# Performance work log

Hardware: AMD Instinct MI355X
Metric: run time of the kernel (lower is better)

Reference implementation:

```python
import jax, jax.numpy as jnp
import numpy as np

B, S, H, K, L, NH, FF = 4, 2048, 2048, 1024, 2, 16, 4096
EPS = 1e-5

def _alibi_slopes(n):
    # standard power-of-two ALiBi slopes
    start = 2.0 ** (-8.0 / n)
    return start ** jnp.arange(1, n + 1, dtype=jnp.float32)

def _layernorm(h, g, b):
    mu = jnp.mean(h, axis=-1, keepdims=True)
    var = jnp.mean(jnp.square(h - mu), axis=-1, keepdims=True)
    return (h - mu) * jax.lax.rsqrt(var + EPS) * g + b

def setup_inputs() -> dict:
    key = jax.random.key(0)
    ks = jax.random.split(key, 16)
    x = jax.random.normal(ks[0], (B, S, H), jnp.float32)
    prev = jax.random.normal(ks[1], (B, S, H), jnp.float32)
    # unique sorted token indices per batch row (jit-friendly boolean mask)
    idx = jnp.stack([jnp.sort(jax.random.permutation(jax.random.fold_in(ks[2], b), S)[:K])
                     for b in range(B)]).astype(jnp.int32)
    w = 0.02
    Wq = jax.random.normal(ks[3], (L, H, H), jnp.float32) * w
    Wk = jax.random.normal(ks[4], (L, H, H), jnp.float32) * w
    Wv = jax.random.normal(ks[5], (L, H, H), jnp.float32) * w
    Wo = jax.random.normal(ks[6], (L, H, H), jnp.float32) * w
    attn_gamma = jnp.ones((L, H), jnp.float32)
    attn_beta = jnp.zeros((L, H), jnp.float32)
    mlp_gamma = jnp.ones((L, H), jnp.float32)
    mlp_beta = jnp.zeros((L, H), jnp.float32)
    Wgate = jax.random.normal(ks[7], (L, H, FF), jnp.float32) * w
    Wup = jax.random.normal(ks[8], (L, H, FF), jnp.float32) * w
    Wdown = jax.random.normal(ks[9], (L, FF, H), jnp.float32) * w
    return {"x": x, "prev": prev, "idx": idx, "Wq": Wq, "Wk": Wk, "Wv": Wv,
            "Wo": Wo, "attn_gamma": attn_gamma, "attn_beta": attn_beta,
            "mlp_gamma": mlp_gamma, "mlp_beta": mlp_beta,
            "Wgate": Wgate, "Wup": Wup, "Wdown": Wdown}

def _forward(x, prev, idx, Wq, Wk, Wv, Wo, attn_gamma, attn_beta,
             mlp_gamma, mlp_beta, Wgate, Wup, Wdown):
    d = H // NH
    scale = 1.0 / jnp.sqrt(jnp.asarray(d, jnp.float32))
    # gather selected tokens: [B, K, H]
    cur = jnp.take_along_axis(x, idx[:, :, None], axis=1)
    mem = jnp.take_along_axis(prev, idx[:, :, None], axis=1)
    # non-causal ALiBi bias over selected-sequence positions: [NH, K, K]
    pos = jnp.arange(K)
    dist = jnp.abs(pos[:, None] - pos[None, :]).astype(jnp.float32)
    bias = -_alibi_slopes(NH)[:, None, None] * dist
    for l in range(L):
        q = (cur @ Wq[l]).reshape(B, K, NH, d)
        k = (mem @ Wk[l]).reshape(B, K, NH, d)
        v = (mem @ Wv[l]).reshape(B, K, NH, d)
        scores = jnp.einsum('bqhd,bkhd->bhqk', q, k) * scale + bias
        attn = jax.nn.softmax(scores, axis=-1)
        o = jnp.einsum('bhqk,bkhd->bqhd', attn, v).reshape(B, K, H) @ Wo[l]
        cur = cur + o
        normed = _layernorm(cur, attn_gamma[l], attn_beta[l])
        mlp = (jax.nn.silu(normed @ Wgate[l]) * (normed @ Wup[l])) @ Wdown[l]
        cur = cur + mlp
        cur = _layernorm(cur, mlp_gamma[l], mlp_beta[l])
    # scatter-add back: out[mask] += update_val
    out = x.at[jnp.arange(B)[:, None], idx].add(cur)
    return out

def reference(x, prev, idx, Wq, Wk, Wv, Wo, attn_gamma, attn_beta,
              mlp_gamma, mlp_beta, Wgate, Wup, Wdown):
    return _forward(x, prev, idx, Wq, Wk, Wv, Wo, attn_gamma, attn_beta,
                    mlp_gamma, mlp_beta, Wgate, Wup, Wdown)
```

## Files before the change

kernel.cpp:

```cpp
#include <hip/hip_runtime.h>
#include <hip/hip_bf16.h>

#define BB 4
#define SS 2048
#define HH 2048
#define KK 1024
#define LL 2
#define NHH 16
#define FFF 4096
#define DD 128

typedef __attribute__((ext_vector_type(8))) short s8v;
typedef __attribute__((ext_vector_type(4))) short s4v;
typedef __attribute__((ext_vector_type(4))) float f4v;

__device__ __forceinline__ short f2bf(float f) {
  unsigned u = __builtin_bit_cast(unsigned, f);
  u += 0x7fffu + ((u >> 16) & 1u);
  return (short)(u >> 16);
}
__device__ __forceinline__ float bf2f(short s) {
  unsigned u = ((unsigned)(unsigned short)s) << 16;
  return __builtin_bit_cast(float, u);
}
__device__ __forceinline__ f4v mfma16(s8v a, s8v b, f4v c) {
  asm("v_mfma_f32_16x16x32_bf16 %0, %1, %2, %0" : "+v"(c) : "v"(a), "v"(b));
  return c;
}
__device__ __forceinline__ void gload_lds16(const void* g, void* l) {
  __builtin_amdgcn_global_load_lds(
      (__attribute__((address_space(1))) void*)g,
      (__attribute__((address_space(3))) void*)l, 16, 0, 0);
}
template <int N>
__device__ __forceinline__ void barrier_cnt() {
  if constexpr (N == 3)
    asm volatile("s_waitcnt vmcnt(3) expcnt(0) lgkmcnt(0)" ::: "memory");
  else
    asm volatile("s_waitcnt vmcnt(0) expcnt(0) lgkmcnt(0)" ::: "memory");
  __builtin_amdgcn_s_barrier();
  asm volatile("" ::: "memory");
}

__global__ __launch_bounds__(256) void wconv(const float* __restrict__ W,
                                             short* __restrict__ Wt,
                                             int Kd, int N) {
  __shared__ short tile[64][65];
  int n0 = blockIdx.x * 64, k0 = blockIdx.y * 64;
  int t = threadIdx.x;
#pragma unroll
  for (int i = 0; i < 16; ++i) {
    int lin = i * 256 + t;
    int r = lin >> 6, c = lin & 63;
    tile[c][r] = f2bf(W[(size_t)(k0 + r) * N + n0 + c]);
  }
  __syncthreads();
#pragma unroll
  for (int i = 0; i < 16; ++i) {
    int lin = i * 256 + t;
    int r = lin >> 6, c = lin & 63;
    Wt[(size_t)(n0 + r) * Kd + k0 + c] = tile[r][c];
  }
}

__global__ __launch_bounds__(256) void gather_rows(
    const float* __restrict__ x, const float* __restrict__ prev,
    const int* __restrict__ idx, float* __restrict__ cur_f,
    short* __restrict__ cur_b, short* __restrict__ mem_b) {
  int r = blockIdx.x;
  int b = r >> 10, kk = r & (KK - 1);
  int src = idx[b * KK + kk];
  const float4* xs = (const float4*)(x + ((size_t)b * SS + src) * HH);
  const float4* ps = (const float4*)(prev + ((size_t)b * SS + src) * HH);
  float4* cf = (float4*)(cur_f + (size_t)r * HH);
  s4v* cb = (s4v*)(cur_b + (size_t)r * HH);
  s4v* mb = (s4v*)(mem_b + (size_t)r * HH);
  int t = threadIdx.x;
#pragma unroll
  for (int i = 0; i < 2; ++i) {
    int c = t + i * 256;
    float4 xv = xs[c], pv = ps[c];
    cf[c] = xv;
    s4v cv, mv;
    cv[0] = f2bf(xv.x); cv[1] = f2bf(xv.y); cv[2] = f2bf(xv.z); cv[3] = f2bf(xv.w);
    mv[0] = f2bf(pv.x); mv[1] = f2bf(pv.y); mv[2] = f2bf(pv.z); mv[3] = f2bf(pv.w);
    cb[c] = cv; mb[c] = mv;
  }
}

template <int EPI>
__global__ __launch_bounds__(512, 2) void g8p(
    const short* __restrict__ A, const short* __restrict__ Bt,
    float* __restrict__ Cf, short* __restrict__ Cb,
    const short* __restrict__ Other, int M, int N, int Kd) {
  __shared__ __align__(16) short smem[3 * 12288];
  const int t = threadIdx.x;
  const int w = t >> 6, l = t & 63;
  const int wr = w >> 2, wc = w & 3;
  const int l15 = l & 15, lh = l >> 4;
  const int koffs = (lh ^ ((l15 >> 1) & 3)) * 8;

  const int gx = gridDim.x, gy = gridDim.y;
  const int nwg = gx * gy;
  const int bid = blockIdx.y * gx + blockIdx.x;
  const int wg = (bid & 7) * (nwg >> 3) + (bid >> 3);
  const int by = wg & (gy - 1);
  const int bx = wg / gy;
  const int rowBase = by * 128, colBase = bx * 256;

  const int ar = t >> 2;
  const int ac = ((t & 3) ^ ((t >> 3) & 3)) * 8;
  const short* gA = A + (size_t)(rowBase + ar) * Kd + ac;
  const short* gB0 = Bt + (size_t)(colBase + ar) * Kd + ac;
  const short* gB1 = gB0 + (size_t)128 * Kd;
  const int lA = t * 8;
  const int lB = 4096 + t * 8;

  auto stage = [&](int bi, int kt) {
    const int k0 = kt * 32;
    short* base = smem + bi * 12288;
    gload_lds16(gA + k0, base + lA);
    gload_lds16(gB0 + k0, base + lB);
    gload_lds16(gB1 + k0, base + lB + 4096);
  };

  f4v acc[4][4];
#pragma unroll
  for (int i = 0; i < 4; ++i)
#pragma unroll
    for (int j = 0; j < 4; ++j) acc[i][j] = (f4v){0.f, 0.f, 0.f, 0.f};

  const int NT = Kd >> 5;
  stage(0, 0);
  stage(1, 1);
  barrier_cnt<3>();

  int cur = 0;
  for (int kt = 0; kt < NT; ++kt) {
    const short* sb = smem + cur * 12288;
    const bool more = (kt + 2 < NT);
    if (more) {
      int nb = cur + 2; if (nb >= 3) nb -= 3;
      stage(nb, kt + 2);
    }
    s8v af[4], bf[4];
#pragma unroll
    for (int mt = 0; mt < 4; ++mt)
      af[mt] = *(const s8v*)(sb + (wr * 64 + mt * 16 + l15) * 32 + koffs);
#pragma unroll
    for (int nt = 0; nt < 4; ++nt)
      bf[nt] = *(const s8v*)(sb + 4096 + (wc * 64 + nt * 16 + l15) * 32 + koffs);
#pragma unroll
    for (int mt = 0; mt < 4; ++mt)
#pragma unroll
      for (int nt = 0; nt < 4; ++nt)
        acc[mt][nt] = mfma16(af[mt], bf[nt], acc[mt][nt]);
    if (more) barrier_cnt<3>(); else barrier_cnt<0>();
    cur = (cur + 1 == 3) ? 0 : cur + 1;
  }

#pragma unroll
  for (int mt = 0; mt < 4; ++mt) {
#pragma unroll
    for (int nt = 0; nt < 4; ++nt) {
#pragma unroll
      for (int rr = 0; rr < 4; ++rr) {
        int row = rowBase + wr * 64 + mt * 16 + (l >> 4) * 4 + rr;
        int col = colBase + wc * 64 + nt * 16 + l15;
        float v = acc[mt][nt][rr];
        if constexpr (EPI == 0) {
          Cb[(size_t)row * N + col] = f2bf(v);
        } else if constexpr (EPI == 1) {
          Cf[(size_t)row * N + col] += v;
        } else if constexpr (EPI == 2) {
          int b = row >> 10, ktok = row & (KK - 1);
          int h = col >> 7, dd = col & (DD - 1);
          Cb[(((size_t)(b * NHH + h)) * DD + dd) * KK + ktok] = f2bf(v);
        } else if constexpr (EPI == 3) {
          float sv = v / (1.f + __expf(-v));
          Cb[(size_t)row * N + col] = f2bf(sv);
        } else {
          float o = bf2f(Other[(size_t)row * N + col]);
          Cb[(size_t)row * N + col] = f2bf(v * o);
        }
      }
    }
  }
}

__global__ __launch_bounds__(256, 2) void attn_fwd(
    const short* __restrict__ qb, const short* __restrict__ kb,
    const short* __restrict__ vT, short* __restrict__ ob) {
  __shared__ __align__(16) short Kl[64 * 136];
  __shared__ __align__(16) short Vl[128 * 72];
  __shared__ __align__(16) short Pl[64 * 72];
  int b = blockIdx.z, h = blockIdx.y, qt = blockIdx.x;
  int t = threadIdx.x, w = t >> 6, l = t & 63, l15 = l & 15, lh = l >> 4;
  float slope = exp2f(-0.5f * (float)(h + 1));
  const float scale = 0.08838834764831845f;

  s8v qf[4];
  int qrowA = qt * 64 + w * 16 + l15;
  const short* qptr = qb + ((size_t)(b * KK + qrowA)) * HH + h * DD + lh * 8;
#pragma unroll
  for (int ks = 0; ks < 4; ++ks) qf[ks] = *(const s8v*)(qptr + ks * 32);

  f4v oacc[8];
#pragma unroll
  for (int i = 0; i < 8; ++i) oacc[i] = (f4v){0.f, 0.f, 0.f, 0.f};
  float m[4], sden[4];
#pragma unroll
  for (int r = 0; r < 4; ++r) { m[r] = -1e30f; sden[r] = 0.f; }
  int qpos_base = qt * 64 + w * 16 + lh * 4;

  for (int kt = 0; kt < KK / 64; ++kt) {
    {
      int rr = t >> 4, cc = (t & 15) * 8;
#pragma unroll
      for (int it = 0; it < 4; ++it) {
        int krow = it * 16 + rr;
        s8v g = *(const s8v*)(kb + ((size_t)(b * KK + kt * 64 + krow)) * HH + h * DD + cc);
        *(s8v*)&Kl[krow * 136 + cc] = g;
      }
      int dr = t >> 3, c2 = (t & 7) * 8;
#pragma unroll
      for (int it = 0; it < 4; ++it) {
        int drow = it * 32 + dr;
        s8v g = *(const s8v*)(vT + (((size_t)(b * NHH + h)) * DD + drow) * KK + kt * 64 + c2);
        *(s8v*)&Vl[drow * 72 + c2] = g;
      }
    }
    __syncthreads();

    f4v sacc[4];
#pragma unroll
    for (int ct = 0; ct < 4; ++ct) sacc[ct] = (f4v){0.f, 0.f, 0.f, 0.f};
#pragma unroll
    for (int ct = 0; ct < 4; ++ct)
#pragma unroll
      for (int ks = 0; ks < 4; ++ks) {
        s8v kf = *(const s8v*)&Kl[(ct * 16 + l15) * 136 + ks * 32 + lh * 8];
        sacc[ct] = mfma16(qf[ks], kf, sacc[ct]);
      }

#pragma unroll
    for (int r = 0; r < 4; ++r) {
      int qpos = qpos_base + r;
      float mx = -1e30f;
#pragma unroll
      for (int ct = 0; ct < 4; ++ct) {
        int kpos = kt * 64 + ct * 16 + l15;
        float sv = sacc[ct][r] * scale - slope * fabsf((float)(qpos - kpos));
        sacc[ct][r] = sv;
        mx = fmaxf(mx, sv);
      }
      mx = fmaxf(mx, __shfl_xor(mx, 1));
      mx = fmaxf(mx, __shfl_xor(mx, 2));
      mx = fmaxf(mx, __shfl_xor(mx, 4));
      mx = fmaxf(mx, __shfl_xor(mx, 8));
      float mn = fmaxf(m[r], mx);
      float corr = __expf(m[r] - mn);
      m[r] = mn;
      float ps = 0.f;
#pragma unroll
      for (int ct = 0; ct < 4; ++ct) {
        float p = __expf(sacc[ct][r] - mn);
        sacc[ct][r] = p;
        ps += p;
      }
      ps += __shfl_xor(ps, 1); ps += __shfl_xor(ps, 2);
      ps += __shfl_xor(ps, 4); ps += __shfl_xor(ps, 8);
      sden[r] = sden[r] * corr + ps;
#pragma unroll
      for (int dt = 0; dt < 8; ++dt) oacc[dt][r] *= corr;
#pragma unroll
      for (int ct = 0; ct < 4; ++ct)
        Pl[(w * 16 + lh * 4 + r) * 72 + ct * 16 + l15] = f2bf(sacc[ct][r]);
    }

#pragma unroll
    for (int ks2 = 0; ks2 < 2; ++ks2) {
      s8v pa = *(const s8v*)&Pl[(w * 16 + l15) * 72 + ks2 * 32 + lh * 8];
#pragma unroll
      for (int dt = 0; dt < 8; ++dt) {
        s8v vf = *(const s8v*)&Vl[(dt * 16 + l15) * 72 + ks2 * 32 + lh * 8];
        oacc[dt] = mfma16(pa, vf, oacc[dt]);
      }
    }
    __syncthreads();
  }

#pragma unroll
  for (int dt = 0; dt < 8; ++dt)
#pragma unroll
    for (int r = 0; r < 4; ++r) {
      int qpos = qpos_base + r;
      int dd = dt * 16 + l15;
      ob[((size_t)(b * KK + qpos)) * HH + h * DD + dd] = f2bf(oacc[dt][r] / sden[r]);
    }
}

__global__ __launch_bounds__(256) void ln_rows(const float* in,
    const float* __restrict__ gma, const float* __restrict__ bta,
    short* __restrict__ outb, float* outf) {
  __shared__ float red[2][4];
  int r = blockIdx.x, t = threadIdx.x;
  const float4* x4 = (const float4*)(in + (size_t)r * HH);
  float4 va = x4[t], vb = x4[t + 256];
  float sum = va.x + va.y + va.z + va.w + vb.x + vb.y + vb.z + vb.w;
  float sq = va.x * va.x + va.y * va.y + va.z * va.z + va.w * va.w +
             vb.x * vb.x + vb.y * vb.y + vb.z * vb.z + vb.w * vb.w;
#pragma unroll
  for (int off = 32; off; off >>= 1) {
    sum += __shfl_down(sum, off);
    sq += __shfl_down(sq, off);
  }
  int w = t >> 6;
  if ((t & 63) == 0) { red[0][w] = sum; red[1][w] = sq; }
  __syncthreads();
  sum = red[0][0] + red[0][1] + red[0][2] + red[0][3];
  sq = red[1][0] + red[1][1] + red[1][2] + red[1][3];
  float mu = sum * (1.f / HH);
  float rs = rsqrtf(sq * (1.f / HH) - mu * mu + 1e-5f);
  const float4* g4 = (const float4*)gma;
  const float4* b4 = (const float4*)bta;
  s4v* ob = (s4v*)(outb + (size_t)r * HH);
  float4* of = (float4*)(outf ? outf + (size_t)r * HH : nullptr);
#pragma unroll
  for (int i = 0; i < 2; ++i) {
    int c = t + i * 256;
    float4 v = (i == 0) ? va : vb;
    float4 g = g4[c], bb = b4[c];
    float4 nv;
    nv.x = (v.x - mu) * rs * g.x + bb.x;
    nv.y = (v.y - mu) * rs * g.y + bb.y;
    nv.z = (v.z - mu) * rs * g.z + bb.z;
    nv.w = (v.w - mu) * rs * g.w + bb.w;
    s4v o;
    o[0] = f2bf(nv.x); o[1] = f2bf(nv.y); o[2] = f2bf(nv.z); o[3] = f2bf(nv.w);
    ob[c] = o;
    if (outf) of[c] = nv;
  }
}

__global__ __launch_bounds__(256) void copy_out(const float* __restrict__ x,
                                                float* __restrict__ out, size_t n4) {
  size_t i = (size_t)blockIdx.x * 256 + threadIdx.x;
  size_t stride = (size_t)gridDim.x * 256;
  const float4* xi = (const float4*)x;
  float4* oi = (float4*)out;
  for (; i < n4; i += stride) oi[i] = xi[i];
}

__global__ __launch_bounds__(256) void scatter_add(const int* __restrict__ idx,
                                                   const float* __restrict__ cur,
                                                   float* out) {
  int r = blockIdx.x;
  int b = r >> 10, kk = r & (KK - 1);
  int dst = idx[b * KK + kk];
  float4* o = (float4*)(out + ((size_t)b * SS + dst) * HH);
  const float4* c = (const float4*)(cur + (size_t)r * HH);
  int t = threadIdx.x;
#pragma unroll
  for (int i = 0; i < 2; ++i) {
    int j = t + i * 256;
    float4 ov = o[j], cv = c[j];
    ov.x += cv.x; ov.y += cv.y; ov.z += cv.z; ov.w += cv.w;
    o[j] = ov;
  }
}

extern "C" void kernel_launch(void* const* d_in, const int* in_sizes, int n_in,
                              void* d_out, int out_size, void* d_ws, size_t ws_size,
                              hipStream_t stream) {
  (void)in_sizes; (void)n_in; (void)out_size; (void)ws_size;
  const float* x = (const float*)d_in[0];
  const float* prv = (const float*)d_in[1];
  const int* idx = (const int*)d_in[2];
  const float* Wq = (const float*)d_in[3];
  const float* Wk = (const float*)d_in[4];
  const float* Wv = (const float*)d_in[5];
  const float* Wo = (const float*)d_in[6];
  const float* ag = (const float*)d_in[7];
  const float* ab = (const float*)d_in[8];
  const float* mg = (const float*)d_in[9];
  const float* mbt = (const float*)d_in[10];
  const float* Wg = (const float*)d_in[11];
  const float* Wu = (const float*)d_in[12];
  const float* Wd = (const float*)d_in[13];
  float* out = (float*)d_out;

  char* ws = (char*)d_ws;
  size_t off = 0;
  auto alloc = [&](size_t bytes) -> void* {
    void* p = ws + off;
    off += (bytes + 255) & ~(size_t)255;
    return p;
  };
  const size_t WHH = (size_t)HH * HH, WHF = (size_t)HH * FFF;
  short* WqT = (short*)alloc(LL * WHH * 2);
  short* WkT = (short*)alloc(LL * WHH * 2);
  short* WvT = (short*)alloc(LL * WHH * 2);
  short* WoT = (short*)alloc(LL * WHH * 2);
  short* WgT = (short*)alloc(LL * WHF * 2);
  short* WuT = (short*)alloc(LL * WHF * 2);
  short* WdT = (short*)alloc(LL * WHF * 2);
  const size_t RH = (size_t)BB * KK * HH;
  float* cur_f = (float*)alloc(RH * 4);
  short* q_b = (short*)alloc(RH * 2);
  short* k_b = (short*)alloc(RH * 2);
  short* vT_b = (short*)alloc(RH * 2);
  short* o_b = (short*)alloc(RH * 2);
  short* cur_b = (short*)alloc(RH * 2);
  short* mem_b = (short*)alloc(RH * 2);
  short* nrm_b = (short*)alloc(RH * 2);
  short* sg_b = q_b;
  short* hid_b = vT_b;

  dim3 blk(256), blk512(512);
  for (int l = 0; l < LL; ++l) {
    wconv<<<dim3(HH / 64, HH / 64), blk, 0, stream>>>(Wq + l * WHH, WqT + l * WHH, HH, HH);
    wconv<<<dim3(HH / 64, HH / 64), blk, 0, stream>>>(Wk + l * WHH, WkT + l * WHH, HH, HH);
    wconv<<<dim3(HH / 64, HH / 64), blk, 0, stream>>>(Wv + l * WHH, WvT + l * WHH, HH, HH);
    wconv<<<dim3(HH / 64, HH / 64), blk, 0, stream>>>(Wo + l * WHH, WoT + l * WHH, HH, HH);
    wconv<<<dim3(FFF / 64, HH / 64), blk, 0, stream>>>(Wg + l * WHF, WgT + l * WHF, HH, FFF);
    wconv<<<dim3(FFF / 64, HH / 64), blk, 0, stream>>>(Wu + l * WHF, WuT + l * WHF, HH, FFF);
    wconv<<<dim3(HH / 64, FFF / 64), blk, 0, stream>>>(Wd + l * WHF, WdT + l * WHF, FFF, HH);
  }
  gather_rows<<<dim3(BB * KK), blk, 0, stream>>>(x, prv, idx, cur_f, cur_b, mem_b);

  const int M = BB * KK;
  for (int l = 0; l < LL; ++l) {
    const short* wq = WqT + l * WHH;
    const short* wk = WkT + l * WHH;
    const short* wv = WvT + l * WHH;
    const short* wo = WoT + l * WHH;
    const short* wg_ = WgT + l * WHF;
    const short* wu = WuT + l * WHF;
    const short* wd = WdT + l * WHF;
    g8p<0><<<dim3(HH / 256, M / 128), blk512, 0, stream>>>(cur_b, wq, nullptr, q_b, nullptr, M, HH, HH);
    g8p<0><<<dim3(HH / 256, M / 128), blk512, 0, stream>>>(mem_b, wk, nullptr, k_b, nullptr, M, HH, HH);
    g8p<2><<<dim3(HH / 256, M / 128), blk512, 0, stream>>>(mem_b, wv, nullptr, vT_b, nullptr, M, HH, HH);
    attn_fwd<<<dim3(KK / 64, NHH, BB), blk, 0, stream>>>(q_b, k_b, vT_b, o_b);
    g8p<1><<<dim3(HH / 256, M / 128), blk512, 0, stream>>>(o_b, wo, cur_f, nullptr, nullptr, M, HH, HH);
    ln_rows<<<dim3(M), blk, 0, stream>>>(cur_f, ag + l * HH, ab + l * HH, nrm_b, nullptr);
    g8p<3><<<dim3(FFF / 256, M / 128), blk512, 0, stream>>>(nrm_b, wg_, nullptr, sg_b, nullptr, M, FFF, HH);
    g8p<4><<<dim3(FFF / 256, M / 128), blk512, 0, stream>>>(nrm_b, wu, nullptr, hid_b, sg_b, M, FFF, HH);
    g8p<1><<<dim3(HH / 256, M / 128), blk512, 0, stream>>>(hid_b, wd, cur_f, nullptr, nullptr, M, HH, FFF);
    ln_rows<<<dim3(M), blk, 0, stream>>>(cur_f, mg + l * HH, mbt + l * HH, cur_b, cur_f);
  }
  copy_out<<<dim3(2048), blk, 0, stream>>>(x, out, (size_t)BB * SS * HH / 4);
  scatter_add<<<dim3(M), blk, 0, stream>>>(idx, cur_f, out);
}
```

Before: 1.338 ms.

## Add 256x256-tile GEMM for MLP gate/up and lazy-rescale exp2 softmax in attention

Adds a new GEMM kernel with 256x256 output tiles, a three-buffer global-to-LDS pipeline and a remapped workgroup order, and uses it for the two large FFN up-projections. The larger tile is meant to raise arithmetic intensity and cut global and LDS traffic per MFMA, at the cost of more accumulator registers and LDS. Separately, the attention kernel folds log2(e) into the scale and ALiBi slope so it can use exp2, and skips the running-max rescale of the output and denominator when every lane's new max is within 8 of the old one. That skip saves multiplies but allows unrescaled exponents up to 2^8, which is a small numerical risk.

After: 1.448 ms. 8.3% more time.

```diff
diff --git a/kernel.cpp b/kernel.cpp
--- a/kernel.cpp
+++ b/kernel.cpp
@@ -36,6 +36,8 @@
 __device__ __forceinline__ void barrier_cnt() {
   if constexpr (N == 3)
     asm volatile("s_waitcnt vmcnt(3) expcnt(0) lgkmcnt(0)" ::: "memory");
+  else if constexpr (N == 4)
+    asm volatile("s_waitcnt vmcnt(4) expcnt(0) lgkmcnt(0)" ::: "memory");
   else
     asm volatile("s_waitcnt vmcnt(0) expcnt(0) lgkmcnt(0)" ::: "memory");
   __builtin_amdgcn_s_barrier();
@@ -165,7 +167,7 @@
     for (int nt = 0; nt < 4; ++nt) {
 #pragma unroll
       for (int rr = 0; rr < 4; ++rr) {
-        int row = rowBase + wr * 64 + mt * 16 + (l >> 4) * 4 + rr;
+        int row = rowBase + wr * 64 + mt * 16 + lh * 4 + rr;
         int col = colBase + wc * 64 + nt * 16 + l15;
         float v = acc[mt][nt][rr];
         if constexpr (EPI == 0) {
@@ -188,6 +190,102 @@
   }
 }
 
+template <int EPI>
+__global__ __launch_bounds__(512, 2) void g256(
+    const short* __restrict__ A, const short* __restrict__ Bt,
+    float* __restrict__ Cf, short* __restrict__ Cb,
+    const short* __restrict__ Other, int M, int N, int Kd) {
+  __shared__ __align__(16) short smem[3 * 16384];
+  const int t = threadIdx.x;
+  const int w = t >> 6, l = t & 63;
+  const int wr = w >> 1, wc = w & 1;
+  const int l15 = l & 15, lh = l >> 4;
+  const int koffs = (lh ^ ((l15 >> 1) & 3)) * 8;
+
+  const int gx = gridDim.x, gy = gridDim.y;
+  const int nwg = gx * gy;
+  const int bid = blockIdx.y * gx + blockIdx.x;
+  const int wg = (bid & 7) * (nwg >> 3) + (bid >> 3);
+  const int by = wg & (gy - 1);
+  const int bx = wg / gy;
+  const int rowBase = by * 256, colBase = bx * 256;
+
+  const int ar = t >> 2;
+  const int ac = ((t & 3) ^ ((t >> 3) & 3)) * 8;
+  const short* gA = A + (size_t)(rowBase + ar) * Kd + ac;
+  const short* gB = Bt + (size_t)(colBase + ar) * Kd + ac;
+  const int lA = t * 8;
+  const int lB = 8192 + t * 8;
+
+  auto stage = [&](int bi, int kt) {
+    const int k0 = kt * 32;
+    short* base = smem + bi * 16384;
+    gload_lds16(gA + k0, base + lA);
+    gload_lds16(gA + k0 + (size_t)128 * Kd, base + lA + 4096);
+    gload_lds16(gB + k0, base + lB);
+    gload_lds16(gB + k0 + (size_t)128 * Kd, base + lB + 4096);
+  };
+
+  f4v acc[4][8];
+#pragma unroll
+  for (int i = 0; i < 4; ++i)
+#pragma unroll
+    for (int j = 0; j < 8; ++j) acc[i][j] = (f4v){0.f, 0.f, 0.f, 0.f};
+
+  const int NT = Kd >> 5;
+  stage(0, 0);
+  stage(1, 1);
+  barrier_cnt<4>();
+
+  int cur = 0;
+  for (int kt = 0; kt < NT; ++kt) {
+    const short* sb = smem + cur * 16384;
+    const bool more = (kt + 2 < NT);
+    if (more) {
+      int nb = cur + 2; if (nb >= 3) nb -= 3;
+      stage(nb, kt + 2);
+    }
+    s8v af[4], bf[8];
+#pragma unroll
+    for (int mt = 0; mt < 4; ++mt)
+      af[mt] = *(const s8v*)(sb + (wr * 64 + mt * 16 + l15) * 32 + koffs);
+#pragma unroll
+    for (int nt = 0; nt < 8; ++nt)
+      bf[nt] = *(const s8v*)(sb + 8192 + (wc * 128 + nt * 16 + l15) * 32 + koffs);
+#pragma unroll
+    for (int mt = 0; mt < 4; ++mt)
+#pragma unroll
+      for (int nt = 0; nt < 8; ++nt)
+        acc[mt][nt] = mfma16(af[mt], bf[nt], acc[mt][nt]);
+    if (more) barrier_cnt<4>(); else barrier_cnt<0>();
+    cur = (cur + 1 == 3) ? 0 : cur + 1;
+  }
+
+#pragma unroll
+  for (int mt = 0; mt < 4; ++mt) {
+#pragma unroll
+    for (int nt = 0; nt < 8; ++nt) {
+#pragma unroll
+      for (int rr = 0; rr < 4; ++rr) {
+        int row = rowBase + wr * 64 + mt * 16 + lh * 4 + rr;
+        int col = colBase + wc * 128 + nt * 16 + l15;
+        float v = acc[mt][nt][rr];
+        if constexpr (EPI == 0) {
+          Cb[(size_t)row * N + col] = f2bf(v);
+        } else if constexpr (EPI == 1) {
+          Cf[(size_t)row * N + col] += v;
+        } else if constexpr (EPI == 3) {
+          float sv = v / (1.f + __expf(-v));
+          Cb[(size_t)row * N + col] = f2bf(sv);
+        } else if constexpr (EPI == 4) {
+          float o = bf2f(Other[(size_t)row * N + col]);
+          Cb[(size_t)row * N + col] = f2bf(v * o);
+        }
+      }
+    }
+  }
+}
+
 __global__ __launch_bounds__(256, 2) void attn_fwd(
     const short* __restrict__ qb, const short* __restrict__ kb,
     const short* __restrict__ vT, short* __restrict__ ob) {
@@ -196,8 +294,9 @@
   __shared__ __align__(16) short Pl[64 * 72];
   int b = blockIdx.z, h = blockIdx.y, qt = blockIdx.x;
   int t = threadIdx.x, w = t >> 6, l = t & 63, l15 = l & 15, lh = l >> 4;
-  float slope = exp2f(-0.5f * (float)(h + 1));
-  const float scale = 0.08838834764831845f;
+  const float LOG2E = 1.4426950408889634f;
+  float slope2 = exp2f(-0.5f * (float)(h + 1)) * LOG2E;
+  const float c1 = 0.08838834764831845f * LOG2E;
 
   s8v qf[4];
   int qrowA = qt * 64 + w * 16 + l15;
@@ -243,6 +342,7 @@
         sacc[ct] = mfma16(qf[ks], kf, sacc[ct]);
       }
 
+    float mx4[4];
 #pragma unroll
     for (int r = 0; r < 4; ++r) {
       int qpos = qpos_base + r;
@@ -250,7 +350,7 @@
 #pragma unroll
       for (int ct = 0; ct < 4; ++ct) {
         int kpos = kt * 64 + ct * 16 + l15;
-        float sv = sacc[ct][r] * scale - slope * fabsf((float)(qpos - kpos));
+        float sv = sacc[ct][r] * c1 - slope2 * fabsf((float)(qpos - kpos));
         sacc[ct][r] = sv;
         mx = fmaxf(mx, sv);
       }
@@ -258,21 +358,31 @@
       mx = fmaxf(mx, __shfl_xor(mx, 2));
       mx = fmaxf(mx, __shfl_xor(mx, 4));
       mx = fmaxf(mx, __shfl_xor(mx, 8));
-      float mn = fmaxf(m[r], mx);
-      float corr = __expf(m[r] - mn);
-      m[r] = mn;
+      mx4[r] = mx;
+    }
+    bool small = (mx4[0] <= m[0] + 8.f) && (mx4[1] <= m[1] + 8.f) &&
+                 (mx4[2] <= m[2] + 8.f) && (mx4[3] <= m[3] + 8.f);
+    bool skip = __all(small);
+#pragma unroll
+    for (int r = 0; r < 4; ++r) {
+      if (!skip) {
+        float mn = fmaxf(m[r], mx4[r]);
+        float corr = exp2f(m[r] - mn);
+        m[r] = mn;
+        sden[r] *= corr;
+#pragma unroll
+        for (int dt = 0; dt < 8; ++dt) oacc[dt][r] *= corr;
+      }
       float ps = 0.f;
 #pragma unroll
       for (int ct = 0; ct < 4; ++ct) {
-        float p = __expf(sacc[ct][r] - mn);
+        float p = exp2f(sacc[ct][r] - m[r]);
         sacc[ct][r] = p;
         ps += p;
       }
       ps += __shfl_xor(ps, 1); ps += __shfl_xor(ps, 2);
       ps += __shfl_xor(ps, 4); ps += __shfl_xor(ps, 8);
-      sden[r] = sden[r] * corr + ps;
-#pragma unroll
-      for (int dt = 0; dt < 8; ++dt) oacc[dt][r] *= corr;
+      sden[r] += ps;
 #pragma unroll
       for (int ct = 0; ct < 4; ++ct)
         Pl[(w * 16 + lh * 4 + r) * 72 + ct * 16 + l15] = f2bf(sacc[ct][r]);
@@ -444,8 +554,8 @@
     attn_fwd<<<dim3(KK / 64, NHH, BB), blk, 0, stream>>>(q_b, k_b, vT_b, o_b);
     g8p<1><<<dim3(HH / 256, M / 128), blk512, 0, stream>>>(o_b, wo, cur_f, nullptr, nullptr, M, HH, HH);
     ln_rows<<<dim3(M), blk, 0, stream>>>(cur_f, ag + l * HH, ab + l * HH, nrm_b, nullptr);
-    g8p<3><<<dim3(FFF / 256, M / 128), blk512, 0, stream>>>(nrm_b, wg_, nullptr, sg_b, nullptr, M, FFF, HH);
-    g8p<4><<<dim3(FFF / 256, M / 128), blk512, 0, stream>>>(nrm_b, wu, nullptr, hid_b, sg_b, M, FFF, HH);
+    g256<3><<<dim3(FFF / 256, M / 256), blk512, 0, stream>>>(nrm_b, wg_, nullptr, sg_b, nullptr, M, FFF, HH);
+    g256<4><<<dim3(FFF / 256, M / 256), blk512, 0, stream>>>(nrm_b, wu, nullptr, hid_b, sg_b, M, FFF, HH);
     g8p<1><<<dim3(HH / 256, M / 128), blk512, 0, stream>>>(hid_b, wd, cur_f, nullptr, nullptr, M, HH, FFF);
     ln_rows<<<dim3(M), blk, 0, stream>>>(cur_f, mg + l * HH, mbt + l * HH, cur_b, cur_f);
   }
```
